# Kernel optimization log

Hardware: AMD Instinct MI355X
Metric: run time of the kernel (lower is better)

The kernel has to match this reference:

```python
import math
import jax, jax.numpy as jnp
import numpy as np

G, PQ, PV = 12, 4, 8

def setup_inputs() -> dict:
    key = jax.random.key(0)
    ks = jax.random.split(key, 14)
    N, L, Cn, Ce, Ch = 1, 512, 384, 128, 192
    Node = jax.random.normal(ks[0], (N, L, Cn), jnp.float32)
    Edge = jax.random.normal(ks[1], (N, L, L, Ce), jnp.float32)
    # proper rotation matrices via QR of random gaussians
    raw = jax.random.normal(ks[2], (N, L, 3, 3), jnp.float32)
    rots, _ = jnp.linalg.qr(raw)
    trans = jax.random.normal(ks[3], (N, L, 3), jnp.float32) * 10.0
    def lin(k, fan_in, fan_out):
        return jax.random.normal(k, (fan_in, fan_out), jnp.float32) / np.sqrt(fan_in)
    return {
        'Node': Node, 'Edge': Edge, 'rots': rots, 'trans': trans,
        'Wq': lin(ks[4], Cn, Ch), 'Wk': lin(ks[5], Cn, Ch), 'Wv': lin(ks[6], Cn, Ch),
        'Wqv': lin(ks[7], Cn, 3 * G * PQ), 'Wkv': lin(ks[8], Cn, 3 * G * PQ),
        'Wvv': lin(ks[9], Cn, 3 * G * PV), 'Wbias': lin(ks[10], Ce, G),
        'gamma': jnp.zeros((G,), jnp.float32),
        'Wout': lin(ks[11], Ce * G + Ch + G * PV * 4, Cn),
        'bout': jnp.zeros((Cn,), jnp.float32),
    }

def reference(Node, Edge, rots, trans, Wq, Wk, Wv, Wqv, Wkv, Wvv, Wbias, gamma, Wout, bout):
    N, L, Cn = Node.shape
    Ce = Edge.shape[-1]
    Ch = Wq.shape[1]
    ppg = Ch // G
    t = trans / 10.0  # Frame(T.rots, T.trans / 10.0)
    q = (Node @ Wq).reshape(N, L, G, ppg)
    k = (Node @ Wk).reshape(N, L, G, ppg)
    v = (Node @ Wv).reshape(N, L, G, ppg)
    qv = (Node @ Wqv).reshape(N, L, G, PQ, 3)
    kv = (Node @ Wkv).reshape(N, L, G, PQ, 3)
    vv = (Node @ Wvv).reshape(N, L, G, PV, 3)
    apply_frame = lambda p: jnp.einsum('nlij,nlgpj->nlgpi', rots, p) + t[:, :, None, None]
    qv = apply_frame(qv)
    kv = apply_frame(kv)
    vv = apply_frame(vv)
    # pairwise squared point distances, summed over xyz and query points -> [N,L,L,G]
    d = qv[:, :, None] - kv[:, None]
    sq = jnp.sum(d * d, axis=(-1, -2))
    bias = jnp.einsum('nijc,cg->nijg', Edge, Wbias)
    WC = math.sqrt(2.0 / 9.0 / PQ)
    WL = math.sqrt(1.0 / 3.0)
    attn = jnp.einsum('nlgc,nmgc->nlmg', q, k) / math.sqrt(ppg) + bias
    attn = attn - jax.nn.softplus(gamma) * (WC / 2.0) * sq
    attn = jax.nn.softmax(WL * attn, axis=2)  # softmax over key index m
    O_Edge = jnp.einsum('nijg,nijc->nigc', attn, Edge).reshape(N, L, G * Ce)
    O_Node = jnp.einsum('nijg,njgc->nigc', attn, v).reshape(N, L, Ch)
    O_vec = jnp.einsum('nijg,njgpc->nigpc', attn, vv)
    # invert_apply: R^T (x - t)
    O_vec = jnp.einsum('nlji,nlgpj->nlgpi', rots, O_vec - t[:, :, None, None])
    O_norm = jnp.sqrt(jnp.sum(O_vec * O_vec, axis=-1) + 1e-8).reshape(N, L, -1)
    O_vec = O_vec.reshape(N, L, -1)
    feat = jnp.concatenate([O_Edge, O_Node, O_vec, O_norm], axis=-1)
    return feat @ Wout + bout
```

## Files before the change

### kernel.cpp

```cpp
#include <hip/hip_runtime.h>
#include <math.h>

#define LQ 512
#define CN 384
#define CE 128
#define CH 192
#define NG 12
#define PPG 16
#define FEAT 2112
#define NPROJ 1152
#define WLs 0.5773502691896258f

#define WS_RAW  0u
#define WS_QVG  589824u
#define WS_KVT  663552u
#define WS_VVG  737280u
#define WS_QN   884736u
#define WS_KNT  890880u
#define WS_KT   897024u
#define WS_ATT  995328u
#define WS_FEAT 4141056u
#define WS_PART 5222400u
#define WS_PM   5812224u
#define WS_PS   5824512u
#define WS_LGS  5861376u

__global__ __launch_bounds__(256) void k1a_gemm(
    const float* __restrict__ Node,
    const float* __restrict__ Wq, const float* __restrict__ Wk,
    const float* __restrict__ Wv, const float* __restrict__ Wqv,
    const float* __restrict__ Wkv, const float* __restrict__ Wvv,
    float* __restrict__ ws)
{
    __shared__ float As[64][68];
    __shared__ float Bs[64][48];
    const int tid = threadIdx.x;
    const int cb = blockIdx.x % 24;
    const int l0 = (blockIdx.x / 24) * 64;
    const int col0 = cb * 48;

    const float* W; int nc, lc0;
    if (col0 < 192)      { W = Wq;  nc = 192; lc0 = col0; }
    else if (col0 < 384) { W = Wk;  nc = 192; lc0 = col0 - 192; }
    else if (col0 < 576) { W = Wv;  nc = 192; lc0 = col0 - 384; }
    else if (col0 < 720) { W = Wqv; nc = 144; lc0 = col0 - 576; }
    else if (col0 < 864) { W = Wkv; nc = 144; lc0 = col0 - 720; }
    else                 { W = Wvv; nc = 288; lc0 = col0 - 864; }

    const int tx = tid & 15, ty = tid >> 4;
    float acc[4][3];
#pragma unroll
    for (int r = 0; r < 4; ++r)
#pragma unroll
        for (int c = 0; c < 3; ++c) acc[r][c] = 0.f;

    for (int kc = 0; kc < 6; ++kc) {
        __syncthreads();
#pragma unroll
        for (int pass = 0; pass < 4; ++pass) {
            int m = (tid >> 4) + pass * 16;
            int kk = (tid & 15) * 4;
            const float4 a = *(const float4*)(Node + (size_t)(l0 + m) * CN + kc * 64 + kk);
            As[kk + 0][m] = a.x; As[kk + 1][m] = a.y;
            As[kk + 2][m] = a.z; As[kk + 3][m] = a.w;
        }
#pragma unroll
        for (int p = 0; p < 12; ++p) {
            int idx = p * 256 + tid;
            int kk = idx / 48, c = idx - kk * 48;
            Bs[kk][c] = W[(size_t)(kc * 64 + kk) * nc + lc0 + c];
        }
        __syncthreads();
#pragma unroll 8
        for (int kk = 0; kk < 64; ++kk) {
            const float4 av = *(const float4*)&As[kk][tx * 4];
            const float b0 = Bs[kk][ty * 3 + 0];
            const float b1 = Bs[kk][ty * 3 + 1];
            const float b2 = Bs[kk][ty * 3 + 2];
            acc[0][0] = fmaf(av.x, b0, acc[0][0]); acc[0][1] = fmaf(av.x, b1, acc[0][1]); acc[0][2] = fmaf(av.x, b2, acc[0][2]);
            acc[1][0] = fmaf(av.y, b0, acc[1][0]); acc[1][1] = fmaf(av.y, b1, acc[1][1]); acc[1][2] = fmaf(av.y, b2, acc[1][2]);
            acc[2][0] = fmaf(av.z, b0, acc[2][0]); acc[2][1] = fmaf(av.z, b1, acc[2][1]); acc[2][2] = fmaf(av.z, b2, acc[2][2]);
            acc[3][0] = fmaf(av.w, b0, acc[3][0]); acc[3][1] = fmaf(av.w, b1, acc[3][1]); acc[3][2] = fmaf(av.w, b2, acc[3][2]);
        }
    }
    float* raw = ws + WS_RAW;
#pragma unroll
    for (int r = 0; r < 4; ++r)
#pragma unroll
        for (int c = 0; c < 3; ++c)
            raw[(size_t)(l0 + tx * 4 + r) * NPROJ + col0 + ty * 3 + c] = acc[r][c];
    if (col0 >= 192 && col0 < 384) {
#pragma unroll
        for (int r = 0; r < 4; ++r)
#pragma unroll
            for (int c = 0; c < 3; ++c)
                ws[WS_KT + (size_t)(col0 - 192 + ty * 3 + c) * LQ + l0 + tx * 4 + r] = acc[r][c];
    }
}

__global__ __launch_bounds__(256) void k1b_vec(
    const float* __restrict__ rots, const float* __restrict__ trans,
    float* __restrict__ ws)
{
    __shared__ float sqbuf[96];
    const int tid = threadIdx.x;
    const int l = blockIdx.x;
    const float* raw = ws + WS_RAW + (size_t)l * NPROJ;

    if (tid < 192) {
        int src, pt, typ;
        if (tid < 48)      { typ = 0; pt = tid;      src = 576 + pt * 3; }
        else if (tid < 96) { typ = 1; pt = tid - 48; src = 720 + pt * 3; }
        else               { typ = 2; pt = tid - 96; src = 864 + pt * 3; }
        float v0 = raw[src], v1 = raw[src + 1], v2 = raw[src + 2];
        const float* R = rots + l * 9;
        float o0 = R[0] * v0 + R[1] * v1 + R[2] * v2 + trans[l * 3 + 0] * 0.1f;
        float o1 = R[3] * v0 + R[4] * v1 + R[5] * v2 + trans[l * 3 + 1] * 0.1f;
        float o2 = R[6] * v0 + R[7] * v1 + R[8] * v2 + trans[l * 3 + 2] * 0.1f;
        if (typ == 0) {
            float* dst = ws + WS_QVG + (size_t)l * 144 + pt * 3;
            dst[0] = o0; dst[1] = o1; dst[2] = o2;
        } else if (typ == 1) {
            ws[WS_KVT + (size_t)(pt * 3 + 0) * LQ + l] = o0;
            ws[WS_KVT + (size_t)(pt * 3 + 1) * LQ + l] = o1;
            ws[WS_KVT + (size_t)(pt * 3 + 2) * LQ + l] = o2;
        } else {
            float* dst = ws + WS_VVG + (size_t)l * 288 + pt * 3;
            dst[0] = o0; dst[1] = o1; dst[2] = o2;
        }
        if (tid < 96) sqbuf[tid] = o0 * o0 + o1 * o1 + o2 * o2;
    }
    __syncthreads();
    if (tid < 24) {
        int typ = tid / 12, g = tid % 12;
        int b = typ * 48 + g * 4;
        float s = sqbuf[b] + sqbuf[b + 1] + sqbuf[b + 2] + sqbuf[b + 3];
        if (typ == 0) ws[WS_QN + (size_t)l * 12 + g] = s;
        else          ws[WS_KNT + (size_t)g * LQ + l] = s;
    }
}

__global__ __launch_bounds__(256) void k2a_logits(
    const float* __restrict__ gamma, float* __restrict__ ws)
{
    __shared__ float cgls[NG];
    const int tid = threadIdx.x;
    const int i = blockIdx.x >> 1;
    const int h = blockIdx.x & 1;
    const int j = h * 256 + tid;

    if (tid < NG)
        cgls[tid] = log1pf(__expf(gamma[tid])) * 0.11785113019775793f;
    __syncthreads();

    const float* qrow  = ws + WS_RAW + (size_t)i * NPROJ;
    const float* qvrow = ws + WS_QVG + (size_t)i * 144;
    const float* qnrow = ws + WS_QN  + (size_t)i * NG;
    const float* KT  = ws + WS_KT;
    const float* KVT = ws + WS_KVT;
    const float* KNT = ws + WS_KNT;
    float lgs[NG];
#pragma unroll
    for (int g = 0; g < NG; ++g) {
        float qk = 0.f;
#pragma unroll
        for (int u = 0; u < PPG; ++u)
            qk = fmaf(qrow[g * PPG + u], KT[(size_t)(g * PPG + u) * LQ + j], qk);
        float dt = 0.f;
#pragma unroll
        for (int u = 0; u < 12; ++u)
            dt = fmaf(qvrow[g * 12 + u], KVT[(size_t)(g * 12 + u) * LQ + j], dt);
        float sq = qnrow[g] + KNT[(size_t)g * LQ + j] - 2.f * dt;
        lgs[g] = qk * 0.25f - cgls[g] * sq;
    }
    float4* dst = (float4*)(ws + WS_LGS + ((size_t)i * LQ + j) * NG);
    float4 s0, s1, s2;
    s0.x = lgs[0]; s0.y = lgs[1]; s0.z = lgs[2];  s0.w = lgs[3];
    s1.x = lgs[4]; s1.y = lgs[5]; s1.z = lgs[6];  s1.w = lgs[7];
    s2.x = lgs[8]; s2.y = lgs[9]; s2.z = lgs[10]; s2.w = lgs[11];
    dst[0] = s0; dst[1] = s1; dst[2] = s2;
}

__global__ __launch_bounds__(256, 2) void k2b_bias(
    const float* __restrict__ Edge, const float* __restrict__ Wbias,
    float* __restrict__ ws)
{
    __shared__ float et[2][256 * 33];
    __shared__ float red[4][NG];
    const int tid = threadIdx.x;
    const int i = blockIdx.x >> 1;
    const int h = blockIdx.x & 1;
    const int j = h * 256 + tid;
    const int jr = tid >> 3, c4s = tid & 7;

    float lgs[NG];
    {
        const float4* lg4 = (const float4*)(ws + WS_LGS + ((size_t)i * LQ + j) * NG);
        float4 L0 = lg4[0], L1 = lg4[1], L2 = lg4[2];
        lgs[0] = L0.x; lgs[1] = L0.y; lgs[2] = L0.z;  lgs[3] = L0.w;
        lgs[4] = L1.x; lgs[5] = L1.y; lgs[6] = L1.z;  lgs[7] = L1.w;
        lgs[8] = L2.x; lgs[9] = L2.y; lgs[10] = L2.z; lgs[11] = L2.w;
    }

    const float4* e4 = (const float4*)Edge + ((size_t)i * LQ + h * 256) * 32;
    float4 buf[8];

#pragma unroll
    for (int kk = 0; kk < 8; ++kk) {
        int idx = kk * 256 + tid;
        buf[kk] = e4[(size_t)(idx >> 3) * 32 + (idx & 7)];
    }
#pragma unroll
    for (int kk = 0; kk < 8; ++kk) {
        int idx = kk * 256 + tid;
        float* d = et[0] + (idx >> 3) * 33 + (idx & 7) * 4;
        d[0] = buf[kk].x; d[1] = buf[kk].y; d[2] = buf[kk].z; d[3] = buf[kk].w;
    }
    __syncthreads();

    for (int ch = 0; ch < 4; ++ch) {
        if (ch < 3) {
#pragma unroll
            for (int kk = 0; kk < 8; ++kk) {
                int idx = kk * 256 + tid;
                buf[kk] = e4[(size_t)(idx >> 3) * 32 + (ch + 1) * 8 + (idx & 7)];
            }
        }
        const float* wbch = Wbias + ch * 32 * NG;
        const float* r0 = et[ch & 1] + tid * 33;
#pragma unroll 4
        for (int c = 0; c < 32; ++c) {
            float e0 = r0[c];
            const float* wb = wbch + c * NG;
#pragma unroll
            for (int g = 0; g < NG; ++g) lgs[g] = fmaf(e0, wb[g], lgs[g]);
        }
        if (ch < 3) {
#pragma unroll
            for (int kk = 0; kk < 8; ++kk) {
                int idx = kk * 256 + tid;
                float* d = et[(ch + 1) & 1] + (idx >> 3) * 33 + (idx & 7) * 4;
                d[0] = buf[kk].x; d[1] = buf[kk].y; d[2] = buf[kk].z; d[3] = buf[kk].w;
            }
        }
        __syncthreads();
    }

    const int wid = tid >> 6, lane = tid & 63;
    float pm[NG];
#pragma unroll
    for (int g = 0; g < NG; ++g) pm[g] = lgs[g];
#pragma unroll
    for (int g = 0; g < NG; ++g)
        for (int off = 1; off < 64; off <<= 1)
            pm[g] = fmaxf(pm[g], __shfl_xor(pm[g], off));
    if (lane == 0) {
#pragma unroll
        for (int g = 0; g < NG; ++g) red[wid][g] = pm[g];
    }
    __syncthreads();
    float gm[NG];
#pragma unroll
    for (int g = 0; g < NG; ++g)
        gm[g] = fmaxf(fmaxf(red[0][g], red[1][g]), fmaxf(red[2][g], red[3][g]));
    if (tid < NG)
        ws[WS_PM + ((size_t)i * 2 + h) * NG + tid] =
            fmaxf(fmaxf(red[0][tid], red[1][tid]), fmaxf(red[2][tid], red[3][tid]));
    __syncthreads();

    float ps[NG];
#pragma unroll
    for (int g = 0; g < NG; ++g) {
        float e = __expf(WLs * (lgs[g] - gm[g]));
        lgs[g] = e;
        ps[g] = e;
    }
#pragma unroll
    for (int g = 0; g < NG; ++g)
        for (int off = 1; off < 64; off <<= 1)
            ps[g] += __shfl_xor(ps[g], off);
    if (lane == 0) {
#pragma unroll
        for (int g = 0; g < NG; ++g) red[wid][g] = ps[g];
    }
    __syncthreads();
    if (tid < NG)
        ws[WS_PS + ((size_t)i * 2 + h) * NG + tid] =
            red[0][tid] + red[1][tid] + red[2][tid] + red[3][tid];

    float* attT = ws + WS_ATT + (size_t)i * (NG * LQ);
#pragma unroll
    for (int g = 0; g < NG; ++g) attT[g * LQ + j] = lgs[g];
}

__global__ __launch_bounds__(256) void k3a_oedge(
    const float* __restrict__ Edge, float* __restrict__ ws)
{
    __shared__ float atls[NG * 516];
    __shared__ float bufA[4][32][NG][4];
    __shared__ float sc[2][NG];
    const int tid = threadIdx.x;
    const int qi = blockIdx.x;

    if (tid < 24) {
        int hh = tid / NG, g = tid % NG;
        float m0 = ws[WS_PM + ((size_t)qi * 2 + 0) * NG + g];
        float m1 = ws[WS_PM + ((size_t)qi * 2 + 1) * NG + g];
        float ss0 = ws[WS_PS + ((size_t)qi * 2 + 0) * NG + g];
        float ss1 = ws[WS_PS + ((size_t)qi * 2 + 1) * NG + g];
        float m = fmaxf(m0, m1);
        float e0 = __expf(WLs * (m0 - m));
        float e1 = __expf(WLs * (m1 - m));
        float denom = ss0 * e0 + ss1 * e1;
        sc[hh][g] = (hh ? e1 : e0) / denom;
    }
    __syncthreads();

    const float4* attT4 = (const float4*)(ws + WS_ATT + (size_t)qi * (NG * LQ));
#pragma unroll
    for (int m = 0; m < 6; ++m) {
        int idx = m * 256 + tid;
        int g = idx >> 7, j4 = idx & 127;
        float s = sc[j4 >> 6][g];
        float4 v = attT4[g * 128 + j4];
        v.x *= s; v.y *= s; v.z *= s; v.w *= s;
        *(float4*)&atls[g * 516 + j4 * 4] = v;
    }
    __syncthreads();

    const int w = tid >> 6, lane = tid & 63, jh = lane >> 5, c4 = lane & 31;
    float acc[NG][4];
#pragma unroll
    for (int g = 0; g < NG; ++g)
#pragma unroll
        for (int r = 0; r < 4; ++r) acc[g][r] = 0.f;
    const float4* e4 = (const float4*)(Edge + (size_t)qi * LQ * CE);
    for (int s = 0; s < 16; ++s) {
        int j0 = w * 128 + jh * 64 + s * 4;
        float4 e0 = e4[(size_t)(j0 + 0) * 32 + c4];
        float4 e1 = e4[(size_t)(j0 + 1) * 32 + c4];
        float4 e2 = e4[(size_t)(j0 + 2) * 32 + c4];
        float4 e3 = e4[(size_t)(j0 + 3) * 32 + c4];
#pragma unroll
        for (int g = 0; g < NG; ++g) {
            float4 a = *(const float4*)&atls[g * 516 + j0];
            acc[g][0] = fmaf(a.x, e0.x, fmaf(a.y, e1.x, fmaf(a.z, e2.x, fmaf(a.w, e3.x, acc[g][0]))));
            acc[g][1] = fmaf(a.x, e0.y, fmaf(a.y, e1.y, fmaf(a.z, e2.y, fmaf(a.w, e3.y, acc[g][1]))));
            acc[g][2] = fmaf(a.x, e0.z, fmaf(a.y, e1.z, fmaf(a.z, e2.z, fmaf(a.w, e3.z, acc[g][2]))));
            acc[g][3] = fmaf(a.x, e0.w, fmaf(a.y, e1.w, fmaf(a.z, e2.w, fmaf(a.w, e3.w, acc[g][3]))));
        }
    }
#pragma unroll
    for (int g = 0; g < NG; ++g)
#pragma unroll
        for (int r = 0; r < 4; ++r) acc[g][r] += __shfl_xor(acc[g][r], 32);
    if (jh == 0) {
#pragma unroll
        for (int g = 0; g < NG; ++g)
#pragma unroll
            for (int r = 0; r < 4; ++r) bufA[w][c4][g][r] = acc[g][r];
    }
    __syncthreads();
    float* feat = ws + WS_FEAT + (size_t)qi * FEAT;
    for (int m = 0; m < 6; ++m) {
        int o = tid + m * 256;
        int g = o >> 7, c = o & 127;
        int cc4 = c >> 2, r = c & 3;
        feat[o] = bufA[0][cc4][g][r] + bufA[1][cc4][g][r] +
                  bufA[2][cc4][g][r] + bufA[3][cc4][g][r];
    }
}

__global__ __launch_bounds__(256) void k3b_rest(
    const float* __restrict__ rots, const float* __restrict__ trans,
    float* __restrict__ ws)
{
    __shared__ float atls[NG * 516];
    __shared__ float sc[2][NG];
    __shared__ float ovecl[240];
    const int tid = threadIdx.x;
    const int qi = blockIdx.x >> 1;
    const int s  = blockIdx.x & 1;

    if (tid < 24) {
        int hh = tid / NG, g = tid % NG;
        float m0 = ws[WS_PM + ((size_t)qi * 2 + 0) * NG + g];
        float m1 = ws[WS_PM + ((size_t)qi * 2 + 1) * NG + g];
        float ss0 = ws[WS_PS + ((size_t)qi * 2 + 0) * NG + g];
        float ss1 = ws[WS_PS + ((size_t)qi * 2 + 1) * NG + g];
        float m = fmaxf(m0, m1);
        float e0 = __expf(WLs * (m0 - m));
        float e1 = __expf(WLs * (m1 - m));
        float denom = ss0 * e0 + ss1 * e1;
        sc[hh][g] = (hh ? e1 : e0) / denom;
    }
    __syncthreads();

    const float4* attT4 = (const float4*)(ws + WS_ATT + (size_t)qi * (NG * LQ));
#pragma unroll
    for (int m = 0; m < 6; ++m) {
        int idx = m * 256 + tid;
        int g = idx >> 7, j4 = idx & 127;
        float f = sc[j4 >> 6][g];
        float4 v = attT4[g * 128 + j4];
        v.x *= f; v.y *= f; v.z *= f; v.w *= f;
        *(float4*)&atls[g * 516 + j4 * 4] = v;
    }
    __syncthreads();

    float* feat = ws + WS_FEAT + (size_t)qi * FEAT;
    const float* raw = ws + WS_RAW;
    const float* vvg = ws + WS_VVG;
    if (tid < 240) {
        if (s == 0 && tid < 192) {
            int g = tid >> 4;
            const float* arow = atls + g * 516;
            float sum = 0.f;
            for (int j4 = 0; j4 < 128; ++j4) {
                float4 a = *(const float4*)&arow[j4 * 4];
                int j = j4 * 4;
                sum = fmaf(a.x, raw[(size_t)(j + 0) * NPROJ + 384 + tid], sum);
                sum = fmaf(a.y, raw[(size_t)(j + 1) * NPROJ + 384 + tid], sum);
                sum = fmaf(a.z, raw[(size_t)(j + 2) * NPROJ + 384 + tid], sum);
                sum = fmaf(a.w, raw[(size_t)(j + 3) * NPROJ + 384 + tid], sum);
            }
            feat[1536 + tid] = sum;
        } else {
            int u = (s == 0) ? (tid - 192) : (48 + tid);
            int lidx = (s == 0) ? (tid - 192) : tid;
            int g = u / 24;
            const float* arow = atls + g * 516;
            float sum = 0.f;
            for (int j4 = 0; j4 < 128; ++j4) {
                float4 a = *(const float4*)&arow[j4 * 4];
                int j = j4 * 4;
                sum = fmaf(a.x, vvg[(size_t)(j + 0) * 288 + u], sum);
                sum = fmaf(a.y, vvg[(size_t)(j + 1) * 288 + u], sum);
                sum = fmaf(a.z, vvg[(size_t)(j + 2) * 288 + u], sum);
                sum = fmaf(a.w, vvg[(size_t)(j + 3) * 288 + u], sum);
            }
            ovecl[lidx] = sum;
        }
    }
    __syncthreads();

    int npts = (s == 0) ? 16 : 80;
    if (tid < npts) {
        int P = (s == 0) ? tid : (16 + tid);
        int u0l = (s == 0) ? (P * 3) : (P * 3 - 48);
        const float* R = rots + qi * 9;
        float t0 = trans[qi * 3 + 0] * 0.1f;
        float t1 = trans[qi * 3 + 1] * 0.1f;
        float t2 = trans[qi * 3 + 2] * 0.1f;
        float d0 = ovecl[u0l + 0] - t0;
        float d1 = ovecl[u0l + 1] - t1;
        float d2 = ovecl[u0l + 2] - t2;
        float o0 = R[0] * d0 + R[3] * d1 + R[6] * d2;
        float o1 = R[1] * d0 + R[4] * d1 + R[7] * d2;
        float o2 = R[2] * d0 + R[5] * d1 + R[8] * d2;
        feat[1728 + P * 3 + 0] = o0;
        feat[1728 + P * 3 + 1] = o1;
        feat[1728 + P * 3 + 2] = o2;
        feat[2016 + P] = sqrtf(o0 * o0 + o1 * o1 + o2 * o2 + 1e-8f);
    }
}

__global__ __launch_bounds__(256) void k4_gemm(const float* __restrict__ Wout,
                                               float* __restrict__ ws)
{
    __shared__ float As[64][68];
    __shared__ float Bs[64][48];
    const int tid = threadIdx.x;
    const int cc = blockIdx.x >> 6;
    const int t  = blockIdx.x & 63;
    const int l0 = (t >> 3) * 64;
    const int col0 = (t & 7) * 48;
    const float* feat = ws + WS_FEAT;

    const int tx = tid & 15, ty = tid >> 4;
    float acc[4][3];
#pragma unroll
    for (int r = 0; r < 4; ++r)
#pragma unroll
        for (int c = 0; c < 3; ++c) acc[r][c] = 0.f;

    for (int kc = cc * 11; kc < cc * 11 + 11; ++kc) {
        __syncthreads();
#pragma unroll
        for (int pass = 0; pass < 4; ++pass) {
            int m = (tid >> 4) + pass * 16;
            int kk = (tid & 15) * 4;
            const float4 a = *(const float4*)(feat + (size_t)(l0 + m) * FEAT + kc * 64 + kk);
            As[kk + 0][m] = a.x; As[kk + 1][m] = a.y;
            As[kk + 2][m] = a.z; As[kk + 3][m] = a.w;
        }
#pragma unroll
        for (int p = 0; p < 12; ++p) {
            int idx = p * 256 + tid;
            int kk = idx / 48, c = idx - kk * 48;
            Bs[kk][c] = Wout[(size_t)(kc * 64 + kk) * CN + col0 + c];
        }
        __syncthreads();
#pragma unroll 8
        for (int kk = 0; kk < 64; ++kk) {
            const float4 av = *(const float4*)&As[kk][tx * 4];
            const float b0 = Bs[kk][ty * 3 + 0];
            const float b1 = Bs[kk][ty * 3 + 1];
            const float b2 = Bs[kk][ty * 3 + 2];
            acc[0][0] = fmaf(av.x, b0, acc[0][0]); acc[0][1] = fmaf(av.x, b1, acc[0][1]); acc[0][2] = fmaf(av.x, b2, acc[0][2]);
            acc[1][0] = fmaf(av.y, b0, acc[1][0]); acc[1][1] = fmaf(av.y, b1, acc[1][1]); acc[1][2] = fmaf(av.y, b2, acc[1][2]);
            acc[2][0] = fmaf(av.z, b0, acc[2][0]); acc[2][1] = fmaf(av.z, b1, acc[2][1]); acc[2][2] = fmaf(av.z, b2, acc[2][2]);
            acc[3][0] = fmaf(av.w, b0, acc[3][0]); acc[3][1] = fmaf(av.w, b1, acc[3][1]); acc[3][2] = fmaf(av.w, b2, acc[3][2]);
        }
    }
    float* part = ws + WS_PART + (size_t)cc * LQ * CN;
#pragma unroll
    for (int r = 0; r < 4; ++r)
#pragma unroll
        for (int c = 0; c < 3; ++c)
            part[(size_t)(l0 + tx * 4 + r) * CN + col0 + ty * 3 + c] = acc[r][c];
}

__global__ __launch_bounds__(384) void k5_red(const float* __restrict__ bout,
                                              const float* __restrict__ wsc,
                                              float* __restrict__ out)
{
    const int i = blockIdx.x, n = threadIdx.x;
    const float* part = wsc + WS_PART;
    size_t idx = (size_t)i * CN + n;
    size_t st = (size_t)LQ * CN;
    out[idx] = part[idx] + part[st + idx] + part[2 * st + idx] + bout[n];
}

extern "C" void kernel_launch(void* const* d_in, const int* in_sizes, int n_in,
                              void* d_out, int out_size, void* d_ws, size_t ws_size,
                              hipStream_t stream) {
    const float* Node  = (const float*)d_in[0];
    const float* Edge  = (const float*)d_in[1];
    const float* rots  = (const float*)d_in[2];
    const float* trans = (const float*)d_in[3];
    const float* Wq    = (const float*)d_in[4];
    const float* Wk    = (const float*)d_in[5];
    const float* Wv    = (const float*)d_in[6];
    const float* Wqv   = (const float*)d_in[7];
    const float* Wkv   = (const float*)d_in[8];
    const float* Wvv   = (const float*)d_in[9];
    const float* Wbias = (const float*)d_in[10];
    const float* gamma = (const float*)d_in[11];
    const float* Wout  = (const float*)d_in[12];
    const float* bout  = (const float*)d_in[13];
    float* ws = (float*)d_ws;

    k1a_gemm<<<192, 256, 0, stream>>>(Node, Wq, Wk, Wv, Wqv, Wkv, Wvv, ws);
    k1b_vec<<<512, 256, 0, stream>>>(rots, trans, ws);
    k2a_logits<<<1024, 256, 0, stream>>>(gamma, ws);
    k2b_bias<<<1024, 256, 0, stream>>>(Edge, Wbias, ws);
    k3a_oedge<<<512, 256, 0, stream>>>(Edge, ws);
    k3b_rest<<<1024, 256, 0, stream>>>(rots, trans, ws);
    k4_gemm<<<192, 256, 0, stream>>>(Wout, ws);
    k5_red<<<512, 384, 0, stream>>>(bout, ws, (float*)d_out);
}
```

Measured before the change: 208.0 us.

## Transpose Wbias once and single-buffer Edge tile in bias kernel for occupancy

Adds a tiny kernel that writes a [G][Ce] transposed copy of Wbias into the workspace. The bias kernel can then read each group's weights as contiguous float4 vectors, and it accumulates 16 channels at a time from registers. The shared Edge tile goes from double to single buffering, with an extra barrier, and launch bounds rise to 4 blocks per CU. This aims to cut scalar weight loads and raise occupancy in the Edge-streaming bias pass, at the cost of one extra launch, more sync, and less overlap between loads and compute.

```diff
diff --git a/kernel.cpp b/kernel.cpp
--- a/kernel.cpp
+++ b/kernel.cpp
@@ -23,7 +23,18 @@
 #define WS_PART 5222400u
 #define WS_PM   5812224u
 #define WS_PS   5824512u
+#define WS_WBT  5836800u
 #define WS_LGS  5861376u
+
+__global__ __launch_bounds__(256) void k0_wbt(const float* __restrict__ Wbias,
+                                              float* __restrict__ ws)
+{
+    int idx = blockIdx.x * 256 + threadIdx.x;
+    if (idx < CE * NG) {
+        int c = idx / NG, g = idx % NG;
+        ws[WS_WBT + g * CE + c] = Wbias[idx];
+    }
+}
 
 __global__ __launch_bounds__(256) void k1a_gemm(
     const float* __restrict__ Node,
@@ -181,17 +192,15 @@
     dst[0] = s0; dst[1] = s1; dst[2] = s2;
 }
 
-__global__ __launch_bounds__(256, 2) void k2b_bias(
-    const float* __restrict__ Edge, const float* __restrict__ Wbias,
-    float* __restrict__ ws)
-{
-    __shared__ float et[2][256 * 33];
+__global__ __launch_bounds__(256, 4) void k2b_bias(
+    const float* __restrict__ Edge, float* __restrict__ ws)
+{
+    __shared__ float et[256 * 33];
     __shared__ float red[4][NG];
     const int tid = threadIdx.x;
     const int i = blockIdx.x >> 1;
     const int h = blockIdx.x & 1;
     const int j = h * 256 + tid;
-    const int jr = tid >> 3, c4s = tid & 7;
 
     float lgs[NG];
     {
@@ -202,6 +211,7 @@
         lgs[8] = L2.x; lgs[9] = L2.y; lgs[10] = L2.z; lgs[11] = L2.w;
     }
 
+    const float* wbT = ws + WS_WBT;
     const float4* e4 = (const float4*)Edge + ((size_t)i * LQ + h * 256) * 32;
     float4 buf[8];
 
@@ -213,7 +223,7 @@
 #pragma unroll
     for (int kk = 0; kk < 8; ++kk) {
         int idx = kk * 256 + tid;
-        float* d = et[0] + (idx >> 3) * 33 + (idx & 7) * 4;
+        float* d = et + (idx >> 3) * 33 + (idx & 7) * 4;
         d[0] = buf[kk].x; d[1] = buf[kk].y; d[2] = buf[kk].z; d[3] = buf[kk].w;
     }
     __syncthreads();
@@ -226,20 +236,34 @@
                 buf[kk] = e4[(size_t)(idx >> 3) * 32 + (ch + 1) * 8 + (idx & 7)];
             }
         }
-        const float* wbch = Wbias + ch * 32 * NG;
-        const float* r0 = et[ch & 1] + tid * 33;
-#pragma unroll 4
-        for (int c = 0; c < 32; ++c) {
-            float e0 = r0[c];
-            const float* wb = wbch + c * NG;
-#pragma unroll
-            for (int g = 0; g < NG; ++g) lgs[g] = fmaf(e0, wb[g], lgs[g]);
-        }
+        const float* r0 = et + tid * 33;
+#pragma unroll
+        for (int hf = 0; hf < 2; ++hf) {
+            float ev[16];
+#pragma unroll
+            for (int c = 0; c < 16; ++c) ev[c] = r0[hf * 16 + c];
+#pragma unroll
+            for (int g = 0; g < NG; ++g) {
+                const float4* wg = (const float4*)(wbT + g * CE + ch * 32 + hf * 16);
+                float4 w0 = wg[0], w1 = wg[1], w2 = wg[2], w3 = wg[3];
+                float s = lgs[g];
+                s = fmaf(ev[0],  w0.x, s); s = fmaf(ev[1],  w0.y, s);
+                s = fmaf(ev[2],  w0.z, s); s = fmaf(ev[3],  w0.w, s);
+                s = fmaf(ev[4],  w1.x, s); s = fmaf(ev[5],  w1.y, s);
+                s = fmaf(ev[6],  w1.z, s); s = fmaf(ev[7],  w1.w, s);
+                s = fmaf(ev[8],  w2.x, s); s = fmaf(ev[9],  w2.y, s);
+                s = fmaf(ev[10], w2.z, s); s = fmaf(ev[11], w2.w, s);
+                s = fmaf(ev[12], w3.x, s); s = fmaf(ev[13], w3.y, s);
+                s = fmaf(ev[14], w3.z, s); s = fmaf(ev[15], w3.w, s);
+                lgs[g] = s;
+            }
+        }
+        __syncthreads();
         if (ch < 3) {
 #pragma unroll
             for (int kk = 0; kk < 8; ++kk) {
                 int idx = kk * 256 + tid;
-                float* d = et[(ch + 1) & 1] + (idx >> 3) * 33 + (idx & 7) * 4;
+                float* d = et + (idx >> 3) * 33 + (idx & 7) * 4;
                 d[0] = buf[kk].x; d[1] = buf[kk].y; d[2] = buf[kk].z; d[3] = buf[kk].w;
             }
         }
@@ -551,10 +575,11 @@
     const float* bout  = (const float*)d_in[13];
     float* ws = (float*)d_ws;
 
+    k0_wbt<<<6, 256, 0, stream>>>(Wbias, ws);
     k1a_gemm<<<192, 256, 0, stream>>>(Node, Wq, Wk, Wv, Wqv, Wkv, Wvv, ws);
     k1b_vec<<<512, 256, 0, stream>>>(rots, trans, ws);
     k2a_logits<<<1024, 256, 0, stream>>>(gamma, ws);
-    k2b_bias<<<1024, 256, 0, stream>>>(Edge, Wbias, ws);
+    k2b_bias<<<1024, 256, 0, stream>>>(Edge, ws);
     k3a_oedge<<<512, 256, 0, stream>>>(Edge, ws);
     k3b_rest<<<1024, 256, 0, stream>>>(rots, trans, ws);
     k4_gemm<<<192, 256, 0, stream>>>(Wout, ws);
```

Result: slower. 224.1 us (+7.7%).

## Fuse logit and edge-bias kernels, single-buffer edge tiles for occupancy

Applied to the files above, without the earlier changes.

Merges the QK/point-distance logit kernel into the edge-bias kernel, so logits are computed in registers instead of being written to and re-read from a global scratch buffer. It also drops the double-buffered register prefetch of Edge tiles in favour of a single shared tile with load/sync/compute per chunk, and raises the occupancy hint to 4 blocks per CU. This removes one launch and a round trip of about 12 MB of logits, but the Edge loads no longer overlap with compute within a block, so latency hiding depends on the extra resident blocks.

```diff
diff --git a/kernel.cpp b/kernel.cpp
--- a/kernel.cpp
+++ b/kernel.cpp
@@ -23,7 +23,6 @@
 #define WS_PART 5222400u
 #define WS_PM   5812224u
 #define WS_PS   5824512u
-#define WS_LGS  5861376u
 
 __global__ __launch_bounds__(256) void k1a_gemm(
     const float* __restrict__ Node,
@@ -140,94 +139,59 @@
     }
 }
 
-__global__ __launch_bounds__(256) void k2a_logits(
+__global__ __launch_bounds__(256, 4) void k2_attn(
+    const float* __restrict__ Edge, const float* __restrict__ Wbias,
     const float* __restrict__ gamma, float* __restrict__ ws)
 {
+    __shared__ float et[256 * 33];
     __shared__ float cgls[NG];
-    const int tid = threadIdx.x;
-    const int i = blockIdx.x >> 1;
-    const int h = blockIdx.x & 1;
-    const int j = h * 256 + tid;
-
-    if (tid < NG)
-        cgls[tid] = log1pf(__expf(gamma[tid])) * 0.11785113019775793f;
-    __syncthreads();
-
-    const float* qrow  = ws + WS_RAW + (size_t)i * NPROJ;
-    const float* qvrow = ws + WS_QVG + (size_t)i * 144;
-    const float* qnrow = ws + WS_QN  + (size_t)i * NG;
-    const float* KT  = ws + WS_KT;
-    const float* KVT = ws + WS_KVT;
-    const float* KNT = ws + WS_KNT;
-    float lgs[NG];
-#pragma unroll
-    for (int g = 0; g < NG; ++g) {
-        float qk = 0.f;
-#pragma unroll
-        for (int u = 0; u < PPG; ++u)
-            qk = fmaf(qrow[g * PPG + u], KT[(size_t)(g * PPG + u) * LQ + j], qk);
-        float dt = 0.f;
-#pragma unroll
-        for (int u = 0; u < 12; ++u)
-            dt = fmaf(qvrow[g * 12 + u], KVT[(size_t)(g * 12 + u) * LQ + j], dt);
-        float sq = qnrow[g] + KNT[(size_t)g * LQ + j] - 2.f * dt;
-        lgs[g] = qk * 0.25f - cgls[g] * sq;
-    }
-    float4* dst = (float4*)(ws + WS_LGS + ((size_t)i * LQ + j) * NG);
-    float4 s0, s1, s2;
-    s0.x = lgs[0]; s0.y = lgs[1]; s0.z = lgs[2];  s0.w = lgs[3];
-    s1.x = lgs[4]; s1.y = lgs[5]; s1.z = lgs[6];  s1.w = lgs[7];
-    s2.x = lgs[8]; s2.y = lgs[9]; s2.z = lgs[10]; s2.w = lgs[11];
-    dst[0] = s0; dst[1] = s1; dst[2] = s2;
-}
-
-__global__ __launch_bounds__(256, 2) void k2b_bias(
-    const float* __restrict__ Edge, const float* __restrict__ Wbias,
-    float* __restrict__ ws)
-{
-    __shared__ float et[2][256 * 33];
     __shared__ float red[4][NG];
     const int tid = threadIdx.x;
     const int i = blockIdx.x >> 1;
     const int h = blockIdx.x & 1;
     const int j = h * 256 + tid;
-    const int jr = tid >> 3, c4s = tid & 7;
+
+    if (tid < NG)
+        cgls[tid] = log1pf(__expf(gamma[tid])) * 0.11785113019775793f;
+    __syncthreads();
 
     float lgs[NG];
     {
-        const float4* lg4 = (const float4*)(ws + WS_LGS + ((size_t)i * LQ + j) * NG);
-        float4 L0 = lg4[0], L1 = lg4[1], L2 = lg4[2];
-        lgs[0] = L0.x; lgs[1] = L0.y; lgs[2] = L0.z;  lgs[3] = L0.w;
-        lgs[4] = L1.x; lgs[5] = L1.y; lgs[6] = L1.z;  lgs[7] = L1.w;
-        lgs[8] = L2.x; lgs[9] = L2.y; lgs[10] = L2.z; lgs[11] = L2.w;
+        const float* qrow  = ws + WS_RAW + (size_t)i * NPROJ;
+        const float* qvrow = ws + WS_QVG + (size_t)i * 144;
+        const float* qnrow = ws + WS_QN  + (size_t)i * NG;
+        const float* KT  = ws + WS_KT;
+        const float* KVT = ws + WS_KVT;
+        const float* KNT = ws + WS_KNT;
+#pragma unroll
+        for (int g = 0; g < NG; ++g) {
+            float qk = 0.f;
+#pragma unroll
+            for (int u = 0; u < PPG; ++u)
+                qk = fmaf(qrow[g * PPG + u], KT[(size_t)(g * PPG + u) * LQ + j], qk);
+            float dt = 0.f;
+#pragma unroll
+            for (int u = 0; u < 12; ++u)
+                dt = fmaf(qvrow[g * 12 + u], KVT[(size_t)(g * 12 + u) * LQ + j], dt);
+            float sq = qnrow[g] + KNT[(size_t)g * LQ + j] - 2.f * dt;
+            lgs[g] = qk * 0.25f - cgls[g] * sq;
+        }
     }
 
     const float4* e4 = (const float4*)Edge + ((size_t)i * LQ + h * 256) * 32;
-    float4 buf[8];
-
-#pragma unroll
-    for (int kk = 0; kk < 8; ++kk) {
-        int idx = kk * 256 + tid;
-        buf[kk] = e4[(size_t)(idx >> 3) * 32 + (idx & 7)];
-    }
-#pragma unroll
-    for (int kk = 0; kk < 8; ++kk) {
-        int idx = kk * 256 + tid;
-        float* d = et[0] + (idx >> 3) * 33 + (idx & 7) * 4;
-        d[0] = buf[kk].x; d[1] = buf[kk].y; d[2] = buf[kk].z; d[3] = buf[kk].w;
-    }
-    __syncthreads();
-
     for (int ch = 0; ch < 4; ++ch) {
-        if (ch < 3) {
-#pragma unroll
-            for (int kk = 0; kk < 8; ++kk) {
-                int idx = kk * 256 + tid;
-                buf[kk] = e4[(size_t)(idx >> 3) * 32 + (ch + 1) * 8 + (idx & 7)];
-            }
-        }
+        __syncthreads();
+#pragma unroll
+        for (int kk = 0; kk < 8; ++kk) {
+            int idx = kk * 256 + tid;
+            int jr = idx >> 3, c4 = idx & 7;
+            float4 v = e4[(size_t)jr * 32 + ch * 8 + c4];
+            float* d = et + jr * 33 + c4 * 4;
+            d[0] = v.x; d[1] = v.y; d[2] = v.z; d[3] = v.w;
+        }
+        __syncthreads();
         const float* wbch = Wbias + ch * 32 * NG;
-        const float* r0 = et[ch & 1] + tid * 33;
+        const float* r0 = et + tid * 33;
 #pragma unroll 4
         for (int c = 0; c < 32; ++c) {
             float e0 = r0[c];
@@ -235,15 +199,6 @@
 #pragma unroll
             for (int g = 0; g < NG; ++g) lgs[g] = fmaf(e0, wb[g], lgs[g]);
         }
-        if (ch < 3) {
-#pragma unroll
-            for (int kk = 0; kk < 8; ++kk) {
-                int idx = kk * 256 + tid;
-                float* d = et[(ch + 1) & 1] + (idx >> 3) * 33 + (idx & 7) * 4;
-                d[0] = buf[kk].x; d[1] = buf[kk].y; d[2] = buf[kk].z; d[3] = buf[kk].w;
-            }
-        }
-        __syncthreads();
     }
 
     const int wid = tid >> 6, lane = tid & 63;
@@ -553,8 +508,7 @@
 
     k1a_gemm<<<192, 256, 0, stream>>>(Node, Wq, Wk, Wv, Wqv, Wkv, Wvv, ws);
     k1b_vec<<<512, 256, 0, stream>>>(rots, trans, ws);
-    k2a_logits<<<1024, 256, 0, stream>>>(gamma, ws);
-    k2b_bias<<<1024, 256, 0, stream>>>(Edge, Wbias, ws);
+    k2_attn<<<1024, 256, 0, stream>>>(Edge, Wbias, gamma, ws);
     k3a_oedge<<<512, 256, 0, stream>>>(Edge, ws);
     k3b_rest<<<1024, 256, 0, stream>>>(rots, trans, ws);
     k4_gemm<<<192, 256, 0, stream>>>(Wout, ws);
```

Result: faster. 190.6 us (-8.3%).
